# Kernel optimization log

Measured on AMD Instinct MI355X. Metric: run time of the kernel, lower is better.

## Reference

```python
import jax, jax.numpy as jnp
import numpy as np

NUM_NODES = 9746   # in_c
NUM_USER = 6040
HID_C = 500
OUT_C = 75
NUM_REL = 5
NUM_EDGES = 200000
NUM_BASIS = 2


def setup_inputs() -> dict:
    key = jax.random.key(0)
    ks = jax.random.split(key, 8)
    x = jnp.arange(NUM_NODES, dtype=jnp.int64)
    edge_index = jax.random.randint(ks[0], (2, NUM_EDGES), 0, NUM_NODES, dtype=jnp.int64)
    edge_type = jax.random.randint(ks[1], (NUM_EDGES,), 0, NUM_REL, dtype=jnp.int64)
    edge_norm = jax.random.uniform(ks[2], (NUM_EDGES,), dtype=jnp.float32)
    # learned params (random_init(0.001, .) ~ small uniform init)
    ord_basis = jax.random.normal(ks[3], (NUM_REL, NUM_NODES * HID_C), dtype=jnp.float32) * 0.001
    fc_w = jax.random.normal(ks[4], (OUT_C, HID_C), dtype=jnp.float32) * 0.001
    basis_matrix = jax.random.normal(ks[5], (NUM_BASIS, OUT_C * OUT_C), dtype=jnp.float32) * 0.001
    coefs = jax.random.normal(ks[6], (NUM_REL, NUM_BASIS), dtype=jnp.float32) * 0.001
    return {"x": x, "edge_index": edge_index, "edge_type": edge_type,
            "edge_norm": edge_norm, "ord_basis": ord_basis, "fc_w": fc_w,
            "basis_matrix": basis_matrix, "coefs": coefs}


def reference(x, edge_index, edge_type, edge_norm, ord_basis, fc_w, basis_matrix, coefs):
    # --- RGCLayer: cumulative ordinal basis weights -> gather -> relu -> scale -> scatter-add
    # weight[r] = sum_{r' <= r} ord_basis[r']  (the cat(weight, weight[-1]+basis) loop)
    weight = jnp.cumsum(ord_basis, axis=0).reshape(NUM_REL * NUM_NODES, HID_C)
    # drop_prob = 0 -> node_dropout mask is all ones (identity)
    src, dst = edge_index[0], edge_index[1]
    idx = edge_type * NUM_NODES + x[src]                  # [E] embedding-style index
    msg = jax.nn.relu(weight[idx]) * edge_norm[:, None]    # [E, HID_C]
    feats = jax.ops.segment_sum(msg, dst, num_segments=NUM_NODES)  # [N, HID_C]
    # --- DenseLayer (shared linear, no bias, dropout is identity)
    u = feats[:NUM_USER] @ fc_w.T                          # [U, OUT_C]
    i = feats[NUM_USER:] @ fc_w.T                          # [I, OUT_C]
    # --- BiDecoder: per-relation bilinear score, log_softmax over relations
    Q = jnp.einsum('rb,bf->rf', coefs, basis_matrix).reshape(NUM_REL, OUT_C, OUT_C)
    scores = jnp.einsum('uf,rfg,ig->uir', u, Q, i)         # [U, I, R]
    out = jax.nn.log_softmax(scores.reshape(-1, NUM_REL), axis=1)
    return out
```

## Files before the change

kernel.cpp:

```cpp
#include <hip/hip_runtime.h>

#define NNODES 9746
#define NUSER  6040
#define NITEM  3706
#define HIDC   500
#define OUTC   75
#define NREL   5
#define NEDGES 200000
#define NW     (NNODES * HIDC)

typedef unsigned short u16;
typedef unsigned int   u32;
typedef __attribute__((ext_vector_type(8))) short short8;
typedef __attribute__((ext_vector_type(4))) float f32x4;
typedef __attribute__((ext_vector_type(2))) float f32x2;

__device__ __forceinline__ u16 f2b(float f) {
    union { float f; u32 i; } v; v.f = f;
    u32 r = (v.i + 0x7FFFu + ((v.i >> 16) & 1u)) >> 16;
    return (u16)r;
}
__device__ __forceinline__ u32 pack2(float lo, float hi) {
    return (u32)f2b(lo) | ((u32)f2b(hi) << 16);
}

__global__ __launch_bounds__(256) void k_prep(
        const float* __restrict__ fcw, const float* __restrict__ coefs,
        const float* __restrict__ bm, const int* __restrict__ ei,
        u32* __restrict__ fcwB, float* __restrict__ Q,
        int* __restrict__ cursors, int* __restrict__ bucket) {
    int b = blockIdx.x;
    if (b < 80) {
        int o = b;
        int cp = threadIdx.x;
        float lo = 0.f, hi = 0.f;
        if (o < OUTC) {
            int c0 = 2 * cp;
            if (c0 < HIDC)     lo = fcw[o * HIDC + c0];
            if (c0 + 1 < HIDC) hi = fcw[o * HIDC + c0 + 1];
        }
        fcwB[o * 256 + cp] = pack2(lo, hi);
    } else if (b < 190) {
        int j = (b - 80) * 256 + threadIdx.x;
        if (j < NREL * OUTC * OUTC) {
            int r = j / (OUTC * OUTC);
            int f = j - r * (OUTC * OUTC);
            Q[j] = coefs[2 * r] * bm[f] + coefs[2 * r + 1] * bm[OUTC * OUTC + f];
        }
    } else {
        int e = (b - 190) * 256 + threadIdx.x;
        if (e < NEDGES) {
            int d = ei[NEDGES + e];
            int pos = atomicAdd(&cursors[d], 1);
            if (pos < 64) bucket[d * 64 + pos] = e;
        }
    }
}

#define YBOFF 2560
__global__ __launch_bounds__(320) void k_y(const float* __restrict__ ord,
                                           const u32* __restrict__ fcwB,
                                           float* __restrict__ Y) {
    __shared__ u32 smem[5120];
    const int tid = threadIdx.x;
    const int s0 = blockIdx.x * 16;
    const int wv = tid / 64;
    const int lane = tid & 63;
    const int m = lane & 15;
    const int q = lane >> 4;

    const int as = tid >> 4;
    const int acp = tid & 15;

    f32x4 acc[5];
    #pragma unroll
    for (int r = 0; r < 5; ++r) acc[r] = (f32x4)0.f;

    for (int kc = 0; kc < 16; ++kc) {
        __syncthreads();
        if (tid < 256) {
            int c0 = kc * 32 + 2 * acp;
            float cx = 0.f, cy = 0.f;
            int aoff = as * 32 + 4 * ((acp >> 2) ^ (as & 7)) + (acp & 3);
            bool okc = (c0 < HIDC) && (s0 + as < NNODES);
            const float* op = ord + (size_t)(s0 + as) * HIDC + c0;
            #pragma unroll
            for (int r = 0; r < 5; ++r) {
                if (okc) {
                    float2 v = *(const float2*)(op + (size_t)r * NW);
                    cx += v.x; cy += v.y;
                }
                smem[r * 512 + aoff] = pack2(fmaxf(cx, 0.f), fmaxf(cy, 0.f));
            }
        }
        for (int j = tid; j < 1280; j += 320) {
            int o = j >> 4, cp = j & 15;
            smem[YBOFF + o * 32 + 4 * ((cp >> 2) ^ (o & 7)) + (cp & 3)]
                = fcwB[o * 256 + kc * 16 + cp];
        }
        __syncthreads();

        int co = 4 * (q ^ (m & 7));
        short8 bvv = *(const short8*)&smem[YBOFF + (wv * 16 + m) * 32 + co];
        #pragma unroll
        for (int r = 0; r < 5; ++r) {
            short8 av = *(const short8*)&smem[(r * 16 + m) * 32 + co];
            acc[r] = __builtin_amdgcn_mfma_f32_16x16x32_bf16(av, bvv, acc[r], 0, 0, 0);
        }
    }

    #pragma unroll
    for (int j = 0; j < 4; ++j) {
        int s = s0 + q * 4 + j;
        if (s < NNODES) {
            #pragma unroll
            for (int r = 0; r < 5; ++r)
                Y[((size_t)r * NNODES + s) * 80 + wv * 16 + m] = acc[r][j];
        }
    }
}

__global__ __launch_bounds__(512) void k_ga(
        const int* __restrict__ ei, const int* __restrict__ etype,
        const float* __restrict__ enorm, const float* __restrict__ Y,
        const int* __restrict__ cursors, const int* __restrict__ bucket,
        const float* __restrict__ Q,
        u32* __restrict__ Abf, u32* __restrict__ zbf) {
    __shared__ int   s_src[8][64];
    __shared__ int   s_r[8][64];
    __shared__ float s_n[8][64];
    __shared__ float zs[8][80];
    __shared__ float asf[8][5][80];
    const int tid = threadIdx.x;
    const int w = tid >> 6;
    const int lane = tid & 63;
    const int b = blockIdx.x;
    const int dst = b * 8 + w;

    int deg = (dst < NNODES) ? cursors[dst] : 0;
    if (deg > 64) deg = 64;
    if (lane < deg) {
        int e = bucket[dst * 64 + lane];
        s_src[w][lane] = ei[e];
        s_r[w][lane]   = etype[e];
        s_n[w][lane]   = enorm[e];
    }
    __syncthreads();

    if (lane < 20) {
        float4 acc = make_float4(0.f, 0.f, 0.f, 0.f);
        if (deg > 0) {
            float4 cur = *((const float4*)(Y + ((size_t)s_r[w][0] * NNODES + s_src[w][0]) * 80) + lane);
            for (int p = 1; p < deg; ++p) {
                float4 nxt = *((const float4*)(Y + ((size_t)s_r[w][p] * NNODES + s_src[w][p]) * 80) + lane);
                float nrm = s_n[w][p - 1];
                acc.x += nrm * cur.x; acc.y += nrm * cur.y;
                acc.z += nrm * cur.z; acc.w += nrm * cur.w;
                cur = nxt;
            }
            float nrm = s_n[w][deg - 1];
            acc.x += nrm * cur.x; acc.y += nrm * cur.y;
            acc.z += nrm * cur.z; acc.w += nrm * cur.w;
        }
        *(float4*)&zs[w][lane * 4] = acc;
    }
    __syncthreads();

    if (b < 755) {
        if (tid < NREL * OUTC) {
            int r = tid / OUTC, g = tid - r * OUTC;
            float acc[8] = {};
            for (int f = 0; f < OUTC; ++f) {
                float qv = Q[(r * OUTC + f) * OUTC + g];
                #pragma unroll
                for (int u = 0; u < 8; ++u) acc[u] += zs[u][f] * qv;
            }
            #pragma unroll
            for (int u = 0; u < 8; ++u) asf[u][r][g] = acc[u];
        }
        __syncthreads();
        const int u0 = b * 8;
        for (int j = tid; j < 8 * 5 * 48; j += 512) {
            int u = j / 240; int rem = j - u * 240;
            int r = rem / 48; int wd = rem - r * 48;
            int g0 = 2 * wd;
            float lo = (g0 < OUTC) ? asf[u][r][g0] : 0.f;
            float hi = (g0 + 1 < OUTC) ? asf[u][r][g0 + 1] : 0.f;
            Abf[((size_t)(u0 + u) * 5 + r) * 48 + wd] = pack2(lo, hi);
        }
    } else {
        const int i0 = b * 8 - NUSER;
        for (int j = tid; j < 8 * 48; j += 512) {
            int u = j / 48; int wd = j - u * 48;
            int i = i0 + u;
            if (i < 3712) {
                int g0 = 2 * wd;
                float lo = 0.f, hi = 0.f;
                if (i < NITEM) {
                    if (g0 < OUTC)     lo = zs[u][g0];
                    if (g0 + 1 < OUTC) hi = zs[u][g0 + 1];
                }
                zbf[(size_t)i * 48 + wd] = pack2(lo, hi);
            }
        }
    }
}

#define BOFF 5120
#define OROW 648
__global__ __launch_bounds__(256) void k_scores(const u32* __restrict__ Abf,
                                                const u32* __restrict__ zbf,
                                                float* __restrict__ out) {
    __shared__ u32 smem[13312];
    float* smf = (float*)smem;
    const int tid = threadIdx.x;
    const int utile = blockIdx.x * 16;
    const int itile = blockIdx.y * 128;

    const uint4* Ag = (const uint4*)Abf;
    for (int j = tid; j < 960; j += 256) {
        int u = j / 60; int rem = j - u * 60;
        int r = rem / 12; int w4 = rem - r * 12;
        uint4 v = make_uint4(0u, 0u, 0u, 0u);
        if (utile + u < NUSER) v = Ag[((size_t)(utile + u) * 5 + r) * 12 + w4];
        *(uint4*)&smem[(r * 16 + u) * 64 + 4 * (w4 ^ (u & 7))] = v;
    }
    const uint4* Bg = (const uint4*)zbf;
    for (int j = tid; j < 1536; j += 256) {
        int i = j / 12; int w4 = j - i * 12;
        *(uint4*)&smem[BOFF + i * 64 + 4 * (w4 ^ (i & 7))] = Bg[(size_t)(itile + i) * 12 + w4];
    }
    __syncthreads();

    const int lane = tid & 63;
    const int wv = tid >> 6;
    const int m = lane & 15;
    const int q = lane >> 4;
    const int sw = m & 7;

    f32x4 acc[2][5];
    #pragma unroll
    for (int fi = 0; fi < 2; ++fi)
        #pragma unroll
        for (int r = 0; r < 5; ++r) acc[fi][r] = (f32x4)0.f;

    #pragma unroll
    for (int kc = 0; kc < 3; ++kc) {
        int c = kc * 4 + q;
        int co = 4 * (c ^ sw);
        short8 av[5], bv[2];
        #pragma unroll
        for (int r = 0; r < 5; ++r)
            av[r] = *(const short8*)&smem[(r * 16 + m) * 64 + co];
        #pragma unroll
        for (int fi = 0; fi < 2; ++fi)
            bv[fi] = *(const short8*)&smem[BOFF + (wv * 32 + fi * 16 + m) * 64 + co];
        #pragma unroll
        for (int fi = 0; fi < 2; ++fi)
            #pragma unroll
            for (int r = 0; r < 5; ++r)
                acc[fi][r] = __builtin_amdgcn_mfma_f32_16x16x32_bf16(
                    av[r], bv[fi], acc[fi][r], 0, 0, 0);
    }
    __syncthreads();

    #pragma unroll
    for (int fi = 0; fi < 2; ++fi) {
        int i_loc = wv * 32 + fi * 16 + m;
        #pragma unroll
        for (int j = 0; j < 4; ++j) {
            int u_loc = q * 4 + j;
            float v0 = acc[fi][0][j], v1 = acc[fi][1][j], v2 = acc[fi][2][j],
                  v3 = acc[fi][3][j], v4 = acc[fi][4][j];
            float mx = fmaxf(fmaxf(fmaxf(v0, v1), fmaxf(v2, v3)), v4);
            float ss = __expf(v0 - mx) + __expf(v1 - mx) + __expf(v2 - mx)
                     + __expf(v3 - mx) + __expf(v4 - mx);
            float lse = mx + __logf(ss);
            float* d = smf + u_loc * OROW + 2 * ((utile + u_loc) & 1) + i_loc * 5;
            d[0] = v0 - lse; d[1] = v1 - lse; d[2] = v2 - lse;
            d[3] = v3 - lse; d[4] = v4 - lse;
        }
    }
    __syncthreads();

    int uvalid = NUSER - utile; if (uvalid > 16) uvalid = 16;
    int ivalid = NITEM - itile; if (ivalid > 128) ivalid = 128;
    const int F = ivalid * 5;
    for (int j = tid; j < uvalid * 160; j += 256) {
        int u = j / 160; int k = j - u * 160;
        int sh = (utile + u) & 1;
        int Nq = (F - 2 * sh) >> 2;
        if (k < Nq) {
            size_t gbase = (size_t)(utile + u) * (NITEM * 5) + (size_t)itile * 5;
            f32x4 v = *(const f32x4*)&smf[u * OROW + 4 * sh + 4 * k];
            __builtin_nontemporal_store(v, (f32x4*)(out + gbase + 2 * sh + 4 * k));
        }
    }
    if (tid < uvalid) {
        int u = tid;
        int sh = (utile + u) & 1;
        size_t gbase = (size_t)(utile + u) * (NITEM * 5) + (size_t)itile * 5;
        if (sh) {
            f32x2 h = *(const f32x2*)&smf[u * OROW + 2];
            __builtin_nontemporal_store(h, (f32x2*)(out + gbase));
        }
        int Nq = (F - 2 * sh) >> 2;
        if (((F - 2 * sh) & 3) != 0) {
            int t0 = 2 * sh + 4 * Nq;
            f32x2 tl = *(const f32x2*)&smf[u * OROW + 2 * sh + t0];
            __builtin_nontemporal_store(tl, (f32x2*)(out + gbase + t0));
        }
    }
}

extern "C" void kernel_launch(void* const* d_in, const int* in_sizes, int n_in,
                              void* d_out, int out_size, void* d_ws, size_t ws_size,
                              hipStream_t stream) {
    const int*   ei    = (const int*)d_in[1];
    const int*   etype = (const int*)d_in[2];
    const float* enorm = (const float*)d_in[3];
    const float* ord   = (const float*)d_in[4];
    const float* fcw   = (const float*)d_in[5];
    const float* bm    = (const float*)d_in[6];
    const float* coefs = (const float*)d_in[7];
    float* out = (float*)d_out;

    int*   ws_i    = (int*)d_ws;
    int*   cursors = ws_i + 0;
    int*   bucket  = ws_i + 9748;
    u32*   fcwB    = (u32*)(ws_i + 633496);
    float* Q       = (float*)(ws_i + 653976);
    float* Y       = (float*)(ws_i + 682104);
    u32*   Abf     = (u32*)(ws_i + 4580504);
    u32*   zbf     = (u32*)(ws_i + 6030104);

    (void)hipMemsetAsync(cursors, 0, 9746 * sizeof(int), stream);

    k_prep<<<972, 256, 0, stream>>>(fcw, coefs, bm, ei, fcwB, Q, cursors, bucket);
    k_y<<<(NNODES + 15) / 16, 320, 0, stream>>>(ord, fcwB, Y);
    k_ga<<<1219, 512, 0, stream>>>(ei, etype, enorm, Y, cursors, bucket, Q, Abf, zbf);
    dim3 sg((NUSER + 15) / 16, (NITEM + 127) / 128);
    k_scores<<<sg, 256, 0, stream>>>(Abf, zbf, out);
}
```

Before: 673.1 us.

## Store Y in bf16, prefetch ord loads, split gather across lane groups

The intermediate Y is now stored as bf16 instead of fp32, which halves the bytes written by k_y and read by the edge gather in k_ga. k_y software-prefetches the next chunk of ord into registers while the current chunk is converted and staged in shared memory. The k_ga gather spreads each node's edges over three 20-lane groups and combines them with shuffles, so more lanes of the wave do work. The Q contraction loop is also unrolled by four with float4 shared-memory reads. The cost is reduced precision in Y plus some extra register pressure.

```diff
diff --git a/kernel.cpp b/kernel.cpp
--- a/kernel.cpp
+++ b/kernel.cpp
@@ -60,7 +60,7 @@
 #define YBOFF 2560
 __global__ __launch_bounds__(320) void k_y(const float* __restrict__ ord,
                                            const u32* __restrict__ fcwB,
-                                           float* __restrict__ Y) {
+                                           u16* __restrict__ Ybf) {
     __shared__ u32 smem[5120];
     const int tid = threadIdx.x;
     const int s0 = blockIdx.x * 16;
@@ -76,21 +76,32 @@
     #pragma unroll
     for (int r = 0; r < 5; ++r) acc[r] = (f32x4)0.f;
 
+    const bool ldr = (tid < 256) && (s0 + as < NNODES);
+    const float* op = ord + (size_t)(s0 + as) * HIDC + 2 * acp;
+    const int aoff = as * 32 + 4 * ((acp >> 2) ^ (as & 7)) + (acp & 3);
+
+    float2 v[5];
+    if (ldr) {
+        #pragma unroll
+        for (int r = 0; r < 5; ++r) v[r] = *(const float2*)(op + (size_t)r * NW);
+    }
+
     for (int kc = 0; kc < 16; ++kc) {
         __syncthreads();
         if (tid < 256) {
-            int c0 = kc * 32 + 2 * acp;
+            const int c0 = kc * 32 + 2 * acp;
+            const bool okc = ldr && (c0 < HIDC);
             float cx = 0.f, cy = 0.f;
-            int aoff = as * 32 + 4 * ((acp >> 2) ^ (as & 7)) + (acp & 3);
-            bool okc = (c0 < HIDC) && (s0 + as < NNODES);
-            const float* op = ord + (size_t)(s0 + as) * HIDC + c0;
             #pragma unroll
             for (int r = 0; r < 5; ++r) {
-                if (okc) {
-                    float2 v = *(const float2*)(op + (size_t)r * NW);
-                    cx += v.x; cy += v.y;
-                }
+                if (okc) { cx += v[r].x; cy += v[r].y; }
                 smem[r * 512 + aoff] = pack2(fmaxf(cx, 0.f), fmaxf(cy, 0.f));
+            }
+            const int cnx = (kc + 1) * 32 + 2 * acp;
+            if (ldr && cnx < HIDC) {
+                #pragma unroll
+                for (int r = 0; r < 5; ++r)
+                    v[r] = *(const float2*)(op + (size_t)r * NW + (kc + 1) * 32);
             }
         }
         for (int j = tid; j < 1280; j += 320) {
@@ -115,14 +126,14 @@
         if (s < NNODES) {
             #pragma unroll
             for (int r = 0; r < 5; ++r)
-                Y[((size_t)r * NNODES + s) * 80 + wv * 16 + m] = acc[r][j];
+                Ybf[((size_t)r * NNODES + s) * 80 + wv * 16 + m] = f2b(acc[r][j]);
         }
     }
 }
 
 __global__ __launch_bounds__(512) void k_ga(
         const int* __restrict__ ei, const int* __restrict__ etype,
-        const float* __restrict__ enorm, const float* __restrict__ Y,
+        const float* __restrict__ enorm, const u16* __restrict__ Ybf,
         const int* __restrict__ cursors, const int* __restrict__ bucket,
         const float* __restrict__ Q,
         u32* __restrict__ Abf, u32* __restrict__ zbf) {
@@ -147,36 +158,54 @@
     }
     __syncthreads();
 
+    const int g = lane / 20;
+    const int part = lane - g * 20;
+    float ax = 0.f, ay = 0.f, az = 0.f, aw = 0.f;
+    if (g < 3) {
+        for (int p = g; p < deg; p += 3) {
+            const u16* row = Ybf + ((size_t)s_r[w][p] * NNODES + s_src[w][p]) * 80 + part * 4;
+            uint2 d = *(const uint2*)row;
+            float nrm = s_n[w][p];
+            union { u32 u; float f; } c0, c1, c2, c3;
+            c0.u = d.x << 16; c1.u = d.x & 0xFFFF0000u;
+            c2.u = d.y << 16; c3.u = d.y & 0xFFFF0000u;
+            ax += nrm * c0.f; ay += nrm * c1.f;
+            az += nrm * c2.f; aw += nrm * c3.f;
+        }
+    }
+    ax += __shfl(ax, lane + 20) + __shfl(ax, lane + 40);
+    ay += __shfl(ay, lane + 20) + __shfl(ay, lane + 40);
+    az += __shfl(az, lane + 20) + __shfl(az, lane + 40);
+    aw += __shfl(aw, lane + 20) + __shfl(aw, lane + 40);
     if (lane < 20) {
-        float4 acc = make_float4(0.f, 0.f, 0.f, 0.f);
-        if (deg > 0) {
-            float4 cur = *((const float4*)(Y + ((size_t)s_r[w][0] * NNODES + s_src[w][0]) * 80) + lane);
-            for (int p = 1; p < deg; ++p) {
-                float4 nxt = *((const float4*)(Y + ((size_t)s_r[w][p] * NNODES + s_src[w][p]) * 80) + lane);
-                float nrm = s_n[w][p - 1];
-                acc.x += nrm * cur.x; acc.y += nrm * cur.y;
-                acc.z += nrm * cur.z; acc.w += nrm * cur.w;
-                cur = nxt;
-            }
-            float nrm = s_n[w][deg - 1];
-            acc.x += nrm * cur.x; acc.y += nrm * cur.y;
-            acc.z += nrm * cur.z; acc.w += nrm * cur.w;
-        }
-        *(float4*)&zs[w][lane * 4] = acc;
+        *(float4*)&zs[w][lane * 4] = make_float4(ax, ay, az, aw);
     }
     __syncthreads();
 
     if (b < 755) {
         if (tid < NREL * OUTC) {
-            int r = tid / OUTC, g = tid - r * OUTC;
+            int r = tid / OUTC, gg = tid - r * OUTC;
+            const float* Qrg = Q + r * OUTC * OUTC + gg;
             float acc[8] = {};
-            for (int f = 0; f < OUTC; ++f) {
-                float qv = Q[(r * OUTC + f) * OUTC + g];
+            for (int f0 = 0; f0 < 72; f0 += 4) {
+                float q0 = Qrg[(f0 + 0) * OUTC];
+                float q1 = Qrg[(f0 + 1) * OUTC];
+                float q2 = Qrg[(f0 + 2) * OUTC];
+                float q3 = Qrg[(f0 + 3) * OUTC];
+                #pragma unroll
+                for (int u = 0; u < 8; ++u) {
+                    float4 zv = *(const float4*)&zs[u][f0];
+                    acc[u] += zv.x * q0 + zv.y * q1 + zv.z * q2 + zv.w * q3;
+                }
+            }
+            #pragma unroll
+            for (int f = 72; f < OUTC; ++f) {
+                float qv = Qrg[f * OUTC];
                 #pragma unroll
                 for (int u = 0; u < 8; ++u) acc[u] += zs[u][f] * qv;
             }
             #pragma unroll
-            for (int u = 0; u < 8; ++u) asf[u][r][g] = acc[u];
+            for (int u = 0; u < 8; ++u) asf[u][r][gg] = acc[u];
         }
         __syncthreads();
         const int u0 = b * 8;
@@ -330,15 +359,15 @@
     int*   bucket  = ws_i + 9748;
     u32*   fcwB    = (u32*)(ws_i + 633496);
     float* Q       = (float*)(ws_i + 653976);
-    float* Y       = (float*)(ws_i + 682104);
-    u32*   Abf     = (u32*)(ws_i + 4580504);
-    u32*   zbf     = (u32*)(ws_i + 6030104);
+    u16*   Ybf     = (u16*)(ws_i + 682104);
+    u32*   Abf     = (u32*)(ws_i + 2631304);
+    u32*   zbf     = (u32*)(ws_i + 4080904);
 
     (void)hipMemsetAsync(cursors, 0, 9746 * sizeof(int), stream);
 
     k_prep<<<972, 256, 0, stream>>>(fcw, coefs, bm, ei, fcwB, Q, cursors, bucket);
-    k_y<<<(NNODES + 15) / 16, 320, 0, stream>>>(ord, fcwB, Y);
-    k_ga<<<1219, 512, 0, stream>>>(ei, etype, enorm, Y, cursors, bucket, Q, Abf, zbf);
+    k_y<<<(NNODES + 15) / 16, 320, 0, stream>>>(ord, fcwB, Ybf);
+    k_ga<<<1219, 512, 0, stream>>>(ei, etype, enorm, Ybf, cursors, bucket, Q, Abf, zbf);
     dim3 sg((NUSER + 15) / 16, (NITEM + 127) / 128);
     k_scores<<<sg, 256, 0, stream>>>(Abf, zbf, out);
 }
```

New measurement: 641.5 us. 4.7% less time.
